# Kernel tuning notes

Measured on AMD Instinct MI355X. Metric: run time of the kernel, lower is better.

## Reference

```python
import jax, jax.numpy as jnp
import numpy as np

V = 50000      # vocab_size
E = 300        # EMBED_SIZE
H = 128        # HIDDEN_SIZE // NUM_DIRS
T = 12         # num_tags
SOS = 3
EOS = 4
NEG = -10000.0


def setup_inputs() -> dict:
    key = jax.random.key(0)
    ks = jax.random.split(key, 14)
    B, S = 128, 512
    x = jax.random.randint(ks[0], (B, S), 0, V)
    y0 = jax.random.randint(ks[1], (B, S), 0, T)
    s = 1.0 / np.sqrt(H)
    u = lambda k, shape: jax.random.uniform(k, shape, jnp.float32, -s, s)
    embed = jax.random.normal(ks[2], (V, E), jnp.float32)
    # torch LSTM gate layout: [i, f, g, o] stacked along first dim (4H)
    Wih_f = u(ks[3], (4 * H, E)); Whh_f = u(ks[4], (4 * H, H)); b_f = u(ks[5], (4 * H,)) + u(ks[6], (4 * H,))
    Wih_b = u(ks[7], (4 * H, E)); Whh_b = u(ks[8], (4 * H, H)); b_b = u(ks[9], (4 * H,)) + u(ks[10], (4 * H,))
    Wout = u(ks[11], (T, 2 * H)); bout = u(ks[12], (T,))
    trans = jax.random.normal(ks[13], (T, T), jnp.float32)
    trans = trans.at[SOS, :].set(NEG).at[:, EOS].set(NEG)
    return dict(x=x, y0=y0, embed=embed,
                Wih_f=Wih_f, Whh_f=Whh_f, b_f=b_f,
                Wih_b=Wih_b, Whh_b=Whh_b, b_b=b_b,
                Wout=Wout, bout=bout, trans=trans)


def _lstm_dir(emb, Wih, Whh, b):
    # emb: [B, S, E] -> hidden states [B, S, H] for one direction
    B = emb.shape[0]
    def step(carry, x_t):
        h, c = carry
        g = x_t @ Wih.T + h @ Whh.T + b  # [B, 4H]
        i, f, gg, o = jnp.split(g, 4, axis=-1)
        c = jax.nn.sigmoid(f) * c + jax.nn.sigmoid(i) * jnp.tanh(gg)
        h = jax.nn.sigmoid(o) * jnp.tanh(c)
        return (h, c), h
    init = (jnp.zeros((B, H), emb.dtype), jnp.zeros((B, H), emb.dtype))
    _, hs = jax.lax.scan(step, init, jnp.swapaxes(emb, 0, 1))  # hs: [S, B, H]
    return jnp.swapaxes(hs, 0, 1)


def reference(x, y0, embed, Wih_f, Whh_f, b_f, Wih_b, Whh_b, b_b, Wout, bout, trans):
    # ---- lstm: embed -> biLSTM -> linear, emissions y: [B, S, T]
    emb = embed[x]
    hf = _lstm_dir(emb, Wih_f, Whh_f, b_f)
    hb = _lstm_dir(emb[:, ::-1], Wih_b, Whh_b, b_b)[:, ::-1]
    y = jnp.concatenate([hf, hb], axis=-1) @ Wout.T + bout

    B = x.shape[0]
    # ---- CRF partition Z via forward algorithm (trans[i, j] = score j -> i)
    score0 = jnp.full((B, T), NEG, y.dtype).at[:, SOS].set(0.0)
    def step(score, emit_t):
        new = jax.nn.logsumexp(score[:, None, :] + trans[None, :, :], axis=-1) + emit_t
        return new, None
    scoreZ, _ = jax.lax.scan(step, score0, jnp.swapaxes(y, 0, 1))
    Z = jax.nn.logsumexp(scoreZ + trans[EOS][None, :], axis=-1)  # [B]

    # ---- gold path score (vectorized version of crf.score)
    y0p = jnp.concatenate([jnp.full((B, 1), SOS, y0.dtype), y0], axis=1)  # [B, S+1]
    emit = jnp.take_along_axis(y, y0p[:, 1:, None], axis=2)[..., 0].sum(axis=1)
    tr = trans[y0p[:, 1:], y0p[:, :-1]].sum(axis=1)
    gold = emit + tr + trans[EOS, y0p[:, -1]]

    return Z - gold  # [B] negative log-likelihood per example
```

## Files before the change

### kernel.cpp

```cpp
#include <hip/hip_runtime.h>

typedef unsigned short u16;
typedef __attribute__((ext_vector_type(8))) short short8;
typedef __attribute__((ext_vector_type(4))) float floatx4;

#define SOS 3
#define EOS 4
#define NEGV -10000.0f
#define LOG2E 1.442695041f
#define TWOLOG2E 2.885390082f

__device__ __forceinline__ u16 f2bf(float f) {
  union { float f; unsigned int i; } v; v.f = f;
  unsigned int r = (v.i + 0x7FFFu + ((v.i >> 16) & 1u)) >> 16;
  return (u16)r;
}
__device__ __forceinline__ void gload_lds16(const u16* g, u16* l) {
  __builtin_amdgcn_global_load_lds((const __attribute__((address_space(1))) void*)g,
                                   (__attribute__((address_space(3))) void*)l, 16, 0, 0);
}

__global__ __launch_bounds__(256) void gather_kernel(const float* __restrict__ embed,
                                                     const int* __restrict__ x,
                                                     u16* __restrict__ A) {
  int idx = blockIdx.x * 256 + threadIdx.x;
  int row = idx / 40;
  int c8 = idx - row * 40;
  int col0 = c8 * 8;
  int b = row & 127, t = row >> 7;
  const float* src = embed + (size_t)x[b * 512 + t] * 300 + col0;
  short8 o;
  if (col0 + 8 <= 300) {
    float4 f0 = *(const float4*)(src);
    float4 f1 = *(const float4*)(src + 4);
    o[0] = (short)f2bf(f0.x); o[1] = (short)f2bf(f0.y);
    o[2] = (short)f2bf(f0.z); o[3] = (short)f2bf(f0.w);
    o[4] = (short)f2bf(f1.x); o[5] = (short)f2bf(f1.y);
    o[6] = (short)f2bf(f1.z); o[7] = (short)f2bf(f1.w);
  } else {
    #pragma unroll
    for (int e = 0; e < 8; ++e)
      o[e] = (col0 + e < 300) ? (short)f2bf(src[e]) : (short)0;
  }
  *(short8*)&A[(size_t)row * 320 + col0] = o;
}

__global__ __launch_bounds__(256) void wpack_kernel(const float* __restrict__ Wf,
                                                    const float* __restrict__ Wb,
                                                    u16* __restrict__ Wp) {
  int idx = blockIdx.x * 256 + threadIdx.x;
  int p = idx / 40;
  int c8 = idx - p * 40;
  int col0 = c8 * 8;
  int dd = p >> 9, q = p & 511;
  int j = q >> 2, g = q & 3;
  const float* src = (dd ? Wb : Wf) + (size_t)(g * 128 + j) * 300;
  short8 o;
  #pragma unroll
  for (int e = 0; e < 8; ++e)
    o[e] = (col0 + e < 300) ? (short)f2bf(src[col0 + e]) : (short)0;
  *(short8*)&Wp[(size_t)p * 320 + col0] = o;
}

__global__ __launch_bounds__(256) void gemm_kernel(const u16* __restrict__ A,
                                                   const u16* __restrict__ B,
                                                   const float* __restrict__ bf_,
                                                   const float* __restrict__ bb_,
                                                   u16* __restrict__ G) {
  __shared__ u16 At[2][128 * 32];
  __shared__ u16 Bt[2][128 * 32];
  const int n = blockIdx.x;
  const int xcd = n & 7, rr = n >> 3;
  const int bx = xcd * 64 + (rr >> 3);
  const int by = rr & 7;
  const int tid = threadIdx.x;
  const int lane = tid & 63;
  const int wave = tid >> 6;
  const int wr = wave >> 1, wc = wave & 1;
  const int arow0 = bx * 128;
  const int bcol0 = by * 128;
  floatx4 acc[4][4] = {};
  const int fq = lane >> 4;
  const int fr = lane & 15;
  const int sr = wave * 32 + (lane >> 2);
  const int sc = (lane & 3) * 8;

#define STAGE(BUF_, K0_) { \
    gload_lds16(&A[(size_t)(arow0 + sr) * 320 + (K0_) + sc],      &At[BUF_][wave * 1024]); \
    gload_lds16(&A[(size_t)(arow0 + sr + 16) * 320 + (K0_) + sc], &At[BUF_][wave * 1024 + 512]); \
    gload_lds16(&B[(size_t)(bcol0 + sr) * 320 + (K0_) + sc],      &Bt[BUF_][wave * 1024]); \
    gload_lds16(&B[(size_t)(bcol0 + sr + 16) * 320 + (K0_) + sc], &Bt[BUF_][wave * 1024 + 512]); \
  }

  STAGE(0, 0);
  __builtin_amdgcn_sched_barrier(0);
  asm volatile("s_waitcnt vmcnt(0)" ::: "memory");
  __builtin_amdgcn_sched_barrier(0);
  __builtin_amdgcn_s_barrier();
  __builtin_amdgcn_sched_barrier(0);

  int cur = 0;
  #pragma unroll 1
  for (int ks = 0; ks < 10; ++ks) {
    if (ks < 9) STAGE(cur ^ 1, (ks + 1) * 32);
    short8 af[4], bfr[4];
    #pragma unroll
    for (int mi = 0; mi < 4; ++mi)
      af[mi] = *(const short8*)&At[cur][(wr * 64 + mi * 16 + fr) * 32 + fq * 8];
    #pragma unroll
    for (int ni = 0; ni < 4; ++ni)
      bfr[ni] = *(const short8*)&Bt[cur][(wc * 64 + ni * 16 + fr) * 32 + fq * 8];
    #pragma unroll
    for (int mi = 0; mi < 4; ++mi)
      #pragma unroll
      for (int ni = 0; ni < 4; ++ni)
        acc[mi][ni] = __builtin_amdgcn_mfma_f32_16x16x32_bf16(bfr[ni], af[mi], acc[mi][ni], 0, 0, 0);
    __builtin_amdgcn_sched_barrier(0);
    asm volatile("s_waitcnt vmcnt(0)" ::: "memory");
    __builtin_amdgcn_sched_barrier(0);
    __builtin_amdgcn_s_barrier();
    __builtin_amdgcn_sched_barrier(0);
    cur ^= 1;
  }
#undef STAGE

  #pragma unroll
  for (int ni = 0; ni < 4; ++ni) {
    const int colq = bcol0 + wc * 64 + ni * 16 + fq * 4;
    const int jj = (colq & 511) >> 2;
    const float* bsrc = (colq >= 512) ? bb_ : bf_;
    const float b0 = bsrc[jj], b1 = bsrc[128 + jj], b2 = bsrc[256 + jj], b3 = bsrc[384 + jj];
    #pragma unroll
    for (int mi = 0; mi < 4; ++mi) {
      const int row = arow0 + wr * 64 + mi * 16 + fr;
      unsigned q0 = f2bf(acc[mi][ni][0] + b0);
      unsigned q1 = f2bf(acc[mi][ni][1] + b1);
      unsigned q2 = f2bf(acc[mi][ni][2] + b2);
      unsigned q3 = f2bf(acc[mi][ni][3] + b3);
      uint2 pk;
      pk.x = q0 | (q1 << 16);
      pk.y = q2 | (q3 << 16);
      *(uint2*)&G[(size_t)row * 1024 + colq] = pk;
    }
  }
}

__global__ __launch_bounds__(512, 2) void lstm_fused_kernel(const u16* __restrict__ Gp,
                                                            const float* __restrict__ Whh_f,
                                                            const float* __restrict__ Whh_b,
                                                            u16* __restrict__ hs) {
  const int bid = blockIdx.x;
  const int d  = bid >> 5;
  const int b0 = (bid & 31) * 4;
  const int tid = threadIdx.x;
  const int w = tid >> 6, lane = tid & 63;
  const int fr = lane & 15, fq = lane >> 4;
  const float* Wd = d ? Whh_b : Whh_f;

  short8 Wfr[4][4];
  #pragma unroll
  for (int tt = 0; tt < 4; ++tt) {
    const int orow = (fr & 3) * 128 + (16 * w + 4 * tt + (fr >> 2));
    #pragma unroll
    for (int kk = 0; kk < 4; ++kk) {
      const float* src = Wd + (size_t)orow * 128 + fq * 8 + kk * 32;
      float4 x0 = *(const float4*)src;
      float4 x1 = *(const float4*)(src + 4);
      short8 o;
      o[0] = (short)f2bf(x0.x); o[1] = (short)f2bf(x0.y);
      o[2] = (short)f2bf(x0.z); o[3] = (short)f2bf(x0.w);
      o[4] = (short)f2bf(x1.x); o[5] = (short)f2bf(x1.y);
      o[6] = (short)f2bf(x1.z); o[7] = (short)f2bf(x1.w);
      Wfr[tt][kk] = o;
    }
  }

  __shared__ __align__(16) u16 hbuf[2][512];
  for (int i = tid; i < 1024; i += 512) (&hbuf[0][0])[i] = 0;
  __syncthreads();

  const int ts = d ? -1 : 1;
  const int t0 = d ? 511 : 0;
  const int bb  = fr & 3;
  const int ttl = fr >> 2;
  const int jj  = 16 * w + 4 * ttl + fq;

  const int ho0 = bb * 128 + (((fq      + 4 * bb) & 15) << 3);
  const int ho1 = bb * 128 + (((fq + 4  + 4 * bb) & 15) << 3);
  const int ho2 = bb * 128 + (((fq + 8  + 4 * bb) & 15) << 3);
  const int ho3 = bb * 128 + (((fq + 12 + 4 * bb) & 15) << 3);
  const int hwi = bb * 128 + ((((jj >> 3) + 4 * bb) & 15) << 3) + (jj & 7);

  const long long gstep = (long long)ts * 131072;
  const long long hstep = (long long)ts * 256;
  const u16* gld = Gp + (long long)t0 * 131072 + (b0 + bb) * 1024 + d * 512 + 4 * jj;
  u16* hsp = hs + (size_t)(b0 + bb) * 131072 + (long long)t0 * 256 + d * 128 + jj;
  float cst = 0.f;

  uint2 gA, gB, gC;
  gA = *(const uint2*)gld; gld += gstep;
  gB = *(const uint2*)gld; gld += gstep;
  gC = *(const uint2*)gld; gld += gstep;

  u16* hr = &hbuf[0][0];
  u16* hw = &hbuf[1][0];

#define STEPN(GR_, PF_) { \
    short8 f0 = *(const short8*)(hr + ho0); \
    short8 f1 = *(const short8*)(hr + ho1); \
    short8 f2 = *(const short8*)(hr + ho2); \
    short8 f3 = *(const short8*)(hr + ho3); \
    floatx4 a0 = {0.f, 0.f, 0.f, 0.f}; \
    floatx4 a1 = a0, a2 = a0, a3 = a0; \
    a0 = __builtin_amdgcn_mfma_f32_16x16x32_bf16(Wfr[0][0], f0, a0, 0, 0, 0); \
    a1 = __builtin_amdgcn_mfma_f32_16x16x32_bf16(Wfr[1][0], f0, a1, 0, 0, 0); \
    a2 = __builtin_amdgcn_mfma_f32_16x16x32_bf16(Wfr[2][0], f0, a2, 0, 0, 0); \
    a3 = __builtin_amdgcn_mfma_f32_16x16x32_bf16(Wfr[3][0], f0, a3, 0, 0, 0); \
    a0 = __builtin_amdgcn_mfma_f32_16x16x32_bf16(Wfr[0][1], f1, a0, 0, 0, 0); \
    a1 = __builtin_amdgcn_mfma_f32_16x16x32_bf16(Wfr[1][1], f1, a1, 0, 0, 0); \
    a2 = __builtin_amdgcn_mfma_f32_16x16x32_bf16(Wfr[2][1], f1, a2, 0, 0, 0); \
    a3 = __builtin_amdgcn_mfma_f32_16x16x32_bf16(Wfr[3][1], f1, a3, 0, 0, 0); \
    a0 = __builtin_amdgcn_mfma_f32_16x16x32_bf16(Wfr[0][2], f2, a0, 0, 0, 0); \
    a1 = __builtin_amdgcn_mfma_f32_16x16x32_bf16(Wfr[1][2], f2, a1, 0, 0, 0); \
    a2 = __builtin_amdgcn_mfma_f32_16x16x32_bf16(Wfr[2][2], f2, a2, 0, 0, 0); \
    a3 = __builtin_amdgcn_mfma_f32_16x16x32_bf16(Wfr[3][2], f2, a3, 0, 0, 0); \
    a0 = __builtin_amdgcn_mfma_f32_16x16x32_bf16(Wfr[0][3], f3, a0, 0, 0, 0); \
    a1 = __builtin_amdgcn_mfma_f32_16x16x32_bf16(Wfr[1][3], f3, a1, 0, 0, 0); \
    a2 = __builtin_amdgcn_mfma_f32_16x16x32_bf16(Wfr[2][3], f3, a2, 0, 0, 0); \
    a3 = __builtin_amdgcn_mfma_f32_16x16x32_bf16(Wfr[3][3], f3, a3, 0, 0, 0); \
    const bool s0 = (ttl & 1), s1 = (ttl & 2); \
    float p0 = s1 ? (s0 ? a3[0] : a2[0]) : (s0 ? a1[0] : a0[0]); \
    float p1 = s1 ? (s0 ? a3[1] : a2[1]) : (s0 ? a1[1] : a0[1]); \
    float p2 = s1 ? (s0 ? a3[2] : a2[2]) : (s0 ? a1[2] : a0[2]); \
    float p3 = s1 ? (s0 ? a3[3] : a2[3]) : (s0 ? a1[3] : a0[3]); \
    float G0 = __builtin_bit_cast(float, GR_.x << 16); \
    float G1 = __builtin_bit_cast(float, GR_.x & 0xffff0000u); \
    float G2 = __builtin_bit_cast(float, GR_.y << 16); \
    float G3 = __builtin_bit_cast(float, GR_.y & 0xffff0000u); \
    if (PF_) { GR_ = *(const uint2*)gld; gld += gstep; } \
    float i_ = p0 + G0, f_ = p1 + G1, g_ = p2 + G2, o_ = p3 + G3; \
    float p  = __builtin_amdgcn_exp2f(__builtin_amdgcn_fmed3f(g_ * TWOLOG2E, -40.f, 40.f)); \
    float qi = __builtin_amdgcn_exp2f(__builtin_amdgcn_fmed3f(i_ * -LOG2E, -40.f, 40.f)); \
    float qf = __builtin_amdgcn_exp2f(__builtin_amdgcn_fmed3f(f_ * -LOG2E, -40.f, 40.f)); \
    float qo = __builtin_amdgcn_exp2f(__builtin_amdgcn_fmed3f(o_ * -LOG2E, -40.f, 40.f)); \
    float D1 = (1.f + qi) * (p + 1.f); \
    float qf1 = 1.f + qf; \
    float cn = (cst * D1 + (p - 1.f) * qf1) * __builtin_amdgcn_rcpf(qf1 * D1); \
    cst = cn; \
    float v = __builtin_amdgcn_exp2f(__builtin_amdgcn_fmed3f(cn * TWOLOG2E, -40.f, 40.f)); \
    float h = (v - 1.f) * __builtin_amdgcn_rcpf((1.f + qo) * (v + 1.f)); \
    u16 hb = f2bf(h); \
    hw[hwi] = hb; \
    *hsp = hb; \
    hsp += hstep; \
    __builtin_amdgcn_sched_barrier(0); \
    asm volatile("s_waitcnt lgkmcnt(0)"); \
    __builtin_amdgcn_sched_barrier(0); \
    __builtin_amdgcn_s_barrier(); \
    __builtin_amdgcn_sched_barrier(0); \
    u16* tp_ = hr; hr = hw; hw = tp_; \
  }

  #pragma unroll 1
  for (int it = 0; it < 170; ++it) {
    STEPN(gA, true);
    STEPN(gB, true);
    STEPN(gC, true);
  }
  STEPN(gA, false);
  STEPN(gB, false);
#undef STEPN
}

__global__ __launch_bounds__(256) void emis_kernel(const u16* __restrict__ hs,
                                                   const float* __restrict__ Wout,
                                                   const float* __restrict__ bout,
                                                   float* __restrict__ y) {
  __shared__ float Ws[12 * 256];
  __shared__ float bs[12];
  const int tid = threadIdx.x;
  for (int i = tid; i < 12 * 256; i += 256) Ws[i] = Wout[i];
  if (tid < 12) bs[tid] = bout[tid];
  __syncthreads();
  const int wave = tid >> 6, lane = tid & 63;
  const size_t m = (size_t)blockIdx.x * 4 + wave;
  uint2 hv = *(const uint2*)&hs[m * 256 + lane * 4];
  float h0 = __builtin_bit_cast(float, hv.x << 16);
  float h1 = __builtin_bit_cast(float, hv.x & 0xffff0000u);
  float h2 = __builtin_bit_cast(float, hv.y << 16);
  float h3 = __builtin_bit_cast(float, hv.y & 0xffff0000u);
  float p[12];
  #pragma unroll
  for (int tg = 0; tg < 12; ++tg) {
    const float* wv = &Ws[tg * 256 + lane * 4];
    p[tg] = h0 * wv[0] + h1 * wv[1] + h2 * wv[2] + h3 * wv[3];
  }
  #pragma unroll
  for (int off = 32; off; off >>= 1)
    #pragma unroll
    for (int tg = 0; tg < 12; ++tg)
      p[tg] += __shfl_xor(p[tg], off);
  if (lane == 0) {
    #pragma unroll
    for (int tg = 0; tg < 12; ++tg)
      y[m * 12 + tg] = p[tg] + bs[tg];
  }
}

__global__ __launch_bounds__(64) void crf_kernel(const float* __restrict__ y,
                                                 const int* __restrict__ y0,
                                                 const float* __restrict__ trans,
                                                 float* __restrict__ out) {
  const int b = blockIdx.x;
  const int lane = threadIdx.x;
  __shared__ float trs[144];
  for (int i = lane; i < 144; i += 64) trs[i] = trans[i];
  __syncthreads();
  const int row = (lane < 12) ? lane : 0;
  float etr[12];
  #pragma unroll
  for (int j = 0; j < 12; ++j) etr[j] = __expf(trs[row * 12 + j]);
  float etreos = (lane < 12) ? __expf(trs[EOS * 12 + lane]) : 0.f;
  float u = (lane == SOS) ? 1.f : 0.f;
  float base = 0.f;
  const float* yb = y + (size_t)b * 512 * 12;
  float pe0 = __expf(yb[row]);
  float pe1 = __expf(yb[12 + row]);
  for (int t = 0; t < 512; ++t) {
    float pe = pe0;
    pe0 = pe1;
    if (t + 2 < 512) pe1 = __expf(yb[(t + 2) * 12 + row]);
    float U[12];
    #pragma unroll
    for (int j = 0; j < 12; ++j)
      U[j] = __builtin_bit_cast(float, __builtin_amdgcn_readlane(__builtin_bit_cast(int, u), j));
    float m_[12];
    #pragma unroll
    for (int j = 0; j < 12; ++j) m_[j] = etr[j] * U[j];
    float d = (((m_[0] + m_[1]) + (m_[2] + m_[3])) + ((m_[4] + m_[5]) + (m_[6] + m_[7])))
            + ((m_[8] + m_[9]) + (m_[10] + m_[11]));
    float uraw = d * pe;
    float r = __builtin_bit_cast(float, __builtin_amdgcn_readlane(__builtin_bit_cast(int, uraw), 0));
    base += __logf(r);
    u = uraw * __builtin_amdgcn_rcpf(r);
  }
  float vv = (lane < 12) ? u * etreos : 0.f;
  #pragma unroll
  for (int off = 32; off; off >>= 1) vv += __shfl_xor(vv, off);
  const float Z = base + __logf(vv);
  const int* y0b = y0 + (size_t)b * 512;
  float acc = 0.f;
  for (int t = lane; t < 512; t += 64) {
    int cur = y0b[t];
    int prev = t ? y0b[t - 1] : SOS;
    acc += yb[t * 12 + cur] + trs[cur * 12 + prev];
  }
  #pragma unroll
  for (int off = 32; off; off >>= 1) acc += __shfl_xor(acc, off);
  if (lane == 0) {
    float gold = acc + trs[EOS * 12 + y0b[511]];
    out[b] = Z - gold;
  }
}

extern "C" void kernel_launch(void* const* d_in, const int* in_sizes, int n_in,
                              void* d_out, int out_size, void* d_ws, size_t ws_size,
                              hipStream_t stream) {
  (void)in_sizes; (void)n_in; (void)out_size; (void)ws_size;
  const int*   x     = (const int*)d_in[0];
  const int*   y0    = (const int*)d_in[1];
  const float* embed = (const float*)d_in[2];
  const float* Wih_f = (const float*)d_in[3];
  const float* Whh_f = (const float*)d_in[4];
  const float* b_f   = (const float*)d_in[5];
  const float* Wih_b = (const float*)d_in[6];
  const float* Whh_b = (const float*)d_in[7];
  const float* b_b   = (const float*)d_in[8];
  const float* Wout  = (const float*)d_in[9];
  const float* bout  = (const float*)d_in[10];
  const float* trans = (const float*)d_in[11];
  float* out = (float*)d_out;

  char* ws = (char*)d_ws;
  u16*   A  = (u16*)(ws);
  u16*   Wp = (u16*)(ws + 41943040);
  u16*   G  = (u16*)(ws + 42598400);
  u16*   hs = (u16*)(ws + 176816128);
  float* yy = (float*)(ws + 210370560);

  gather_kernel<<<10240, 256, 0, stream>>>(embed, x, A);
  wpack_kernel<<<160, 256, 0, stream>>>(Wih_f, Wih_b, Wp);
  gemm_kernel<<<4096, 256, 0, stream>>>(A, Wp, b_f, b_b, G);
  lstm_fused_kernel<<<64, 512, 0, stream>>>(G, Whh_f, Whh_b, hs);
  emis_kernel<<<16384, 256, 0, stream>>>(hs, Wout, bout, yy);
  crf_kernel<<<128, 64, 0, stream>>>(yy, y0, trans, out);
}
```

Before: 555.9 us.

## Enlarge input-projection GEMM tiles to 256x256 with 8 waves, drop double buffering

Reworks the embedding-projection GEMM from 128x128 tiles with 4 waves and double-buffered LDS to 256x256 tiles with 8 waves and a single LDS buffer guarded by __syncthreads. Each wave now computes 128x64 outputs, which raises reuse of loaded A/B data and cuts global traffic per output. The cost is that loads are no longer overlapped with MFMA work, plus higher register pressure from 32 accumulators and a grid of only 1024 blocks.

```diff
diff --git a/kernel.cpp b/kernel.cpp
--- a/kernel.cpp
+++ b/kernel.cpp
@@ -62,67 +62,52 @@
   *(short8*)&Wp[(size_t)p * 320 + col0] = o;
 }
 
-__global__ __launch_bounds__(256) void gemm_kernel(const u16* __restrict__ A,
-                                                   const u16* __restrict__ B,
-                                                   const float* __restrict__ bf_,
-                                                   const float* __restrict__ bb_,
-                                                   u16* __restrict__ G) {
-  __shared__ u16 At[2][128 * 32];
-  __shared__ u16 Bt[2][128 * 32];
+__global__ __launch_bounds__(512, 2) void gemm_kernel(const u16* __restrict__ A,
+                                                      const u16* __restrict__ B,
+                                                      const float* __restrict__ bf_,
+                                                      const float* __restrict__ bb_,
+                                                      u16* __restrict__ G) {
+  __shared__ u16 At[256 * 32];
+  __shared__ u16 Bt[256 * 32];
   const int n = blockIdx.x;
   const int xcd = n & 7, rr = n >> 3;
-  const int bx = xcd * 64 + (rr >> 3);
-  const int by = rr & 7;
+  const int bx = xcd * 32 + (rr >> 2);
+  const int by = rr & 3;
   const int tid = threadIdx.x;
   const int lane = tid & 63;
   const int wave = tid >> 6;
-  const int wr = wave >> 1, wc = wave & 1;
-  const int arow0 = bx * 128;
-  const int bcol0 = by * 128;
-  floatx4 acc[4][4] = {};
+  const int wr = wave >> 2, wc = wave & 3;
+  const int arow0 = bx * 256;
+  const int bcol0 = by * 256;
+  floatx4 acc[8][4] = {};
   const int fq = lane >> 4;
   const int fr = lane & 15;
-  const int sr = wave * 32 + (lane >> 2);
+  const int sr = tid >> 2;
   const int sc = (lane & 3) * 8;
-
-#define STAGE(BUF_, K0_) { \
-    gload_lds16(&A[(size_t)(arow0 + sr) * 320 + (K0_) + sc],      &At[BUF_][wave * 1024]); \
-    gload_lds16(&A[(size_t)(arow0 + sr + 16) * 320 + (K0_) + sc], &At[BUF_][wave * 1024 + 512]); \
-    gload_lds16(&B[(size_t)(bcol0 + sr) * 320 + (K0_) + sc],      &Bt[BUF_][wave * 1024]); \
-    gload_lds16(&B[(size_t)(bcol0 + sr + 16) * 320 + (K0_) + sc], &Bt[BUF_][wave * 1024 + 512]); \
-  }
-
-  STAGE(0, 0);
-  __builtin_amdgcn_sched_barrier(0);
-  asm volatile("s_waitcnt vmcnt(0)" ::: "memory");
-  __builtin_amdgcn_sched_barrier(0);
-  __builtin_amdgcn_s_barrier();
-  __builtin_amdgcn_sched_barrier(0);
-
-  int cur = 0;
+  u16* la = &At[wave * 512 + lane * 8];
+  u16* lb = &Bt[wave * 512 + lane * 8];
+
   #pragma unroll 1
-  for (int ks = 0; ks < 10; ++ks) {
-    if (ks < 9) STAGE(cur ^ 1, (ks + 1) * 32);
-    short8 af[4], bfr[4];
-    #pragma unroll
-    for (int mi = 0; mi < 4; ++mi)
-      af[mi] = *(const short8*)&At[cur][(wr * 64 + mi * 16 + fr) * 32 + fq * 8];
+  for (int k0 = 0; k0 < 320; k0 += 32) {
+    gload_lds16(&A[(size_t)(arow0 + sr) * 320 + k0 + sc],       la);
+    gload_lds16(&A[(size_t)(arow0 + sr + 128) * 320 + k0 + sc], la + 4096);
+    gload_lds16(&B[(size_t)(bcol0 + sr) * 320 + k0 + sc],       lb);
+    gload_lds16(&B[(size_t)(bcol0 + sr + 128) * 320 + k0 + sc], lb + 4096);
+    __syncthreads();
+    short8 af[8], bfr[4];
+    #pragma unroll
+    for (int mi = 0; mi < 8; ++mi)
+      af[mi] = *(const short8*)&At[(wr * 128 + mi * 16 + fr) * 32 + fq * 8];
     #pragma unroll
     for (int ni = 0; ni < 4; ++ni)
-      bfr[ni] = *(const short8*)&Bt[cur][(wc * 64 + ni * 16 + fr) * 32 + fq * 8];
-    #pragma unroll
-    for (int mi = 0; mi < 4; ++mi)
+      bfr[ni] = *(const short8*)&Bt[(wc * 64 + ni * 16 + fr) * 32 + fq * 8];
+    #pragma unroll
+    for (int mi = 0; mi < 8; ++mi)
       #pragma unroll
       for (int ni = 0; ni < 4; ++ni)
         acc[mi][ni] = __builtin_amdgcn_mfma_f32_16x16x32_bf16(bfr[ni], af[mi], acc[mi][ni], 0, 0, 0);
-    __builtin_amdgcn_sched_barrier(0);
-    asm volatile("s_waitcnt vmcnt(0)" ::: "memory");
-    __builtin_amdgcn_sched_barrier(0);
-    __builtin_amdgcn_s_barrier();
-    __builtin_amdgcn_sched_barrier(0);
-    cur ^= 1;
-  }
-#undef STAGE
+    __syncthreads();
+  }
 
   #pragma unroll
   for (int ni = 0; ni < 4; ++ni) {
@@ -131,8 +116,8 @@
     const float* bsrc = (colq >= 512) ? bb_ : bf_;
     const float b0 = bsrc[jj], b1 = bsrc[128 + jj], b2 = bsrc[256 + jj], b3 = bsrc[384 + jj];
     #pragma unroll
-    for (int mi = 0; mi < 4; ++mi) {
-      const int row = arow0 + wr * 64 + mi * 16 + fr;
+    for (int mi = 0; mi < 8; ++mi) {
+      const int row = arow0 + wr * 128 + mi * 16 + fr;
       unsigned q0 = f2bf(acc[mi][ni][0] + b0);
       unsigned q1 = f2bf(acc[mi][ni][1] + b1);
       unsigned q2 = f2bf(acc[mi][ni][2] + b2);
@@ -390,7 +375,7 @@
 
   gather_kernel<<<10240, 256, 0, stream>>>(embed, x, A);
   wpack_kernel<<<160, 256, 0, stream>>>(Wih_f, Wih_b, Wp);
-  gemm_kernel<<<4096, 256, 0, stream>>>(A, Wp, b_f, b_b, G);
+  gemm_kernel<<<1024, 512, 0, stream>>>(A, Wp, b_f, b_b, G);
   lstm_fused_kernel<<<64, 512, 0, stream>>>(G, Whh_f, Whh_b, hs);
   emis_kernel<<<16384, 256, 0, stream>>>(hs, Wout, bout, yy);
   crf_kernel<<<128, 64, 0, stream>>>(yy, y0, trans, out);
```

New measurement: 581.1 us. 1.05x slower.
